# Kernel optimization log

Hardware: AMD Instinct MI355X
Metric: run time of the kernel (lower is better)

## Reference

```python
import jax, jax.numpy as jnp
import numpy as np

ALPHA = 200.0      # cfg.TRAIN.VOTING_ALPHA
RHO = 100.0        # ADMM penalty
SIGMA = 1e-3       # ADMM regularization
ITERS = 150        # fixed ADMM iterations


def _admm_qp(Q, q, C, l, u):
    n = Q.shape[0]
    K = Q + SIGMA * jnp.eye(n, dtype=Q.dtype) + RHO * (C.T @ C)
    cf = jax.scipy.linalg.cho_factor(K)
    x0 = jnp.zeros((n,), Q.dtype)
    z0 = jnp.clip(jnp.zeros((C.shape[0],), Q.dtype), l, u)
    y0 = jnp.zeros((C.shape[0],), Q.dtype)

    def step(carry, _):
        x, z, y = carry
        rhs = SIGMA * x - q + C.T @ (RHO * z - y)
        x = jax.scipy.linalg.cho_solve(cf, rhs)
        Cx = C @ x
        z = jnp.clip(Cx + y / RHO, l, u)
        y = y + RHO * (Cx - z)
        return (x, z, y), None

    (x, _, _), _ = jax.lax.scan(step, (x0, z0, y0), None, length=ITERS)
    return x


def _l2n(x, axis):
    return x / jnp.maximum(jnp.linalg.norm(x, axis=axis, keepdims=True), 1e-12)


def _forward(feat_tra, feat_det, iou_mat, W, b):
    n1, d = feat_tra.shape
    n2 = feat_det.shape[0]
    # cross-graph feature update
    Mp0 = feat_tra @ feat_det.T + iou_mat                      # (n1,n2)
    m1 = Mp0 @ feat_det                                        # (n1,d)
    m2 = Mp0.T @ feat_tra                                      # (n2,d)
    lam1 = jax.lax.stop_gradient(jnp.linalg.norm(feat_tra, axis=1, keepdims=True)
                                 / jnp.linalg.norm(m1, axis=1, keepdims=True))
    lam2 = jax.lax.stop_gradient(jnp.linalg.norm(feat_det, axis=1, keepdims=True)
                                 / jnp.linalg.norm(m2, axis=1, keepdims=True))
    e1 = jax.nn.relu((feat_tra + lam1 * m1) @ W.T + b)
    e2 = jax.nn.relu((feat_det + lam2 * m2) @ W.T + b)
    e1 = _l2n(e1, 1)
    e2 = _l2n(e2, 1)
    Mp = e1 @ e2.T                                             # (n1,n2) unary affinity
    P = Mp.T                                                   # (n2,n1)
    # Quadratic affinity: the torch code builds src_tgt[i,j,k,l] = <cat(e1_i,e1_j), cat(e2_k,e2_l)>
    # = Mp[i,k] + Mp[j,l], then gathers M[(a,c),(b,d)] = src_tgt[c,d,a,b]/2 masked by (a!=b)&(c!=d).
    ms = 1.0 - jnp.eye(n1, dtype=Mp.dtype)
    mt = 1.0 - jnp.eye(n2, dtype=Mp.dtype)
    M4 = 0.5 * (P[:, :, None, None] + P[None, None, :, :]) \
         * (mt[:, None, :, None] * ms[None, :, None, :])       # (n2,n1,n2,n1)
    n = n1 * n2
    Q = float((n1 - 1) * (n2 - 1)) * jnp.eye(n, dtype=Mp.dtype) - M4.reshape(n, n)
    q = -P.reshape(-1)                                         # -Mpp
    # equality constraints (square case): column sums and row sums == 1
    A = jnp.concatenate([jnp.kron(jnp.ones((1, n1)), jnp.eye(n2)),
                         jnp.kron(jnp.eye(n1), jnp.ones((1, n2)))], axis=0).astype(Mp.dtype)
    C = jnp.concatenate([jnp.eye(n, dtype=Mp.dtype), A], axis=0)
    l = jnp.concatenate([jnp.zeros((n,), Mp.dtype), jnp.ones((n1 + n2,), Mp.dtype)])
    u = jnp.concatenate([jnp.full((n,), 1e6, Mp.dtype), jnp.ones((n1 + n2,), Mp.dtype)])
    x = _admm_qp(Q, q, C, l, u)
    s = x.reshape(n2, n1).T                                    # (n1,n2)
    s = jnp.clip(s, 0.0, 1.0)                                  # relu(s) - relu(s-1)
    s = jax.nn.softmax(ALPHA * s, axis=-1)                     # Voting layer
    return s[None]                                             # (1,n1,n2)


def setup_inputs() -> dict:
    key = jax.random.key(0)
    k1, k2, k3, k4 = jax.random.split(key, 4)
    n1 = n2 = 64
    d = 512
    feat_tra = jax.random.normal(k1, (n1, d), jnp.float32)
    feat_det = jax.random.normal(k2, (n2, d), jnp.float32)
    iou_mat = jax.random.uniform(k3, (n1, n2), jnp.float32)
    W = jnp.eye(d, dtype=jnp.float32) + 0.01 * jax.random.normal(k4, (d, d), jnp.float32)
    b = jnp.zeros((d,), jnp.float32)
    return {"feat_tra": feat_tra, "feat_det": feat_det, "iou_mat": iou_mat, "W": W, "b": b}


def reference(feat_tra, feat_det, iou_mat, W, b):
    return _forward(feat_tra, feat_det, iou_mat, W, b)
```

## Files before the change

### kernel.cpp

```cpp
#include <hip/hip_runtime.h>
#include <math.h>

#define DD 512
#define NS 258
#define NSP 264
#define NWG 64
#define BLK 1024
#define RHO_ 100.0
#define SIG_ 1e-3
#define NITER 150
#define DELTA0 (3969.0 + SIG_ + RHO_)

typedef float v2f __attribute__((ext_vector_type(2)));

#define OFF_E1     512u
#define OFF_SUMS   512u
#define OFF_INV    4608u
#define OFF_E2     262656u
#define OFF_P      524800u
#define OFF_W      557568u
#define OFF_P32    590336u
#define OFF_W32    606720u
#define OFF_KSA    623104u
#define OFF_KSB    1168000u
#define OFF_N32    1712896u

__device__ __forceinline__ int perm258(int i){
  return (i < 128) ? i : (i == 128) ? 256 : (i == 129) ? 257 : (i - 2);
}

template<int CTRL>
__device__ __forceinline__ float dppadd(float v){
  int t = __builtin_amdgcn_mov_dpp(__float_as_int(v), CTRL, 0xF, 0xF, 1);
  return v + __int_as_float(t);
}
template<int CTRL>
__device__ __forceinline__ float dppmax(float v){
  int t = __builtin_amdgcn_mov_dpp(__float_as_int(v), CTRL, 0xF, 0xF, 1);
  return fmaxf(v, __int_as_float(t));
}
__device__ __forceinline__ float sum16(float v){
  v = dppadd<0xB1>(v);
  v = dppadd<0x4E>(v);
  v = dppadd<0x124>(v);
  v = dppadd<0x128>(v);
  return v;
}
__device__ __forceinline__ float wsum64f(float v){
  v = sum16(v);
  v += __shfl_xor(v, 16, 64);
  v += __shfl_xor(v, 32, 64);
  return v;
}
__device__ __forceinline__ float wsum64u(float v){
  v = sum16(v);
  v = dppadd<0x142>(v);
  v = dppadd<0x143>(v);
  return __uint_as_float(__builtin_amdgcn_readlane(__float_as_uint(v), 63));
}
__device__ __forceinline__ float wmax64f(float v){
  v = dppmax<0xB1>(v); v = dppmax<0x4E>(v); v = dppmax<0x124>(v); v = dppmax<0x128>(v);
  v = fmaxf(v, __shfl_xor(v, 16, 64));
  v = fmaxf(v, __shfl_xor(v, 32, 64));
  return v;
}

__device__ __forceinline__ double gsum16d(double v){
  v += __shfl_xor(v, 1, 64);
  v += __shfl_xor(v, 2, 64);
  v += __shfl_xor(v, 4, 64);
  v += __shfl_xor(v, 8, 64);
  return v;
}
__device__ __forceinline__ double wsum64d(double v){
  v = gsum16d(v);
  v += __shfl_xor(v, 16, 64);
  v += __shfl_xor(v, 32, 64);
  return v;
}

__device__ __forceinline__ void decode_idx(int t, int& cls, int& pr, int& ix){
  if (t < 64)       { cls = 1; pr = 1; ix = t; }
  else if (t < 128) { cls = 2; pr = 1; ix = t - 64; }
  else if (t == 128){ cls = 0; pr = 1; ix = 0; }
  else if (t == 129){ cls = 0; pr = 0; ix = 0; }
  else if (t < 194) { cls = 1; pr = 0; ix = t - 130; }
  else              { cls = 2; pr = 0; ix = t - 194; }
}

__device__ __forceinline__ double ksval(int r, int c, const double* __restrict__ p,
                                        const double* __restrict__ w, const double* sumsL){
  int cr, prr, ir, cc, prc, ic;
  decode_idx(r, cr, prr, ir);
  decode_idx(c, cc, prc, ic);
  int m = prr + prc;
  double tval;
  if (cr == 0 && cc == 0)      tval = sumsL[m];
  else if (cr == 0 && cc == 1) tval = sumsL[8 + m*64 + ic];
  else if (cr == 1 && cc == 0) tval = sumsL[8 + m*64 + ir];
  else if (cr == 0 && cc == 2) tval = sumsL[200 + m*64 + ic];
  else if (cr == 2 && cc == 0) tval = sumsL[200 + m*64 + ir];
  else if (cr == 1 && cc == 1) tval = (ir == ic) ? sumsL[8 + m*64 + ir] : 0.0;
  else if (cr == 2 && cc == 2) tval = (ir == ic) ? sumsL[200 + m*64 + ir] : 0.0;
  else if (cr == 1 && cc == 2){
    double wv = w[ic*64 + ir], pv = p[ic*64 + ir];
    tval = (m == 0) ? wv : (m == 1) ? wv*pv : wv*pv*pv;
  } else {
    double wv = w[ir*64 + ic], pv = p[ir*64 + ic];
    tval = (m == 0) ? wv : (m == 1) ? wv*pv : wv*pv*pv;
  }
  double mv2 = 0.0;
  if (cr == 0 && cc == 0 && prr != prc) mv2 = -2.0;
  if (cr != 0 && cr == cc && ir == ic){
    if (prr != prc) mv2 = 2.0;
    else if (prr == 1) mv2 = -4.0 * RHO_;
  }
  return tval + mv2;
}

__global__ __launch_bounds__(BLK) void kp_feat(const float* __restrict__ ft,
                                               const float* __restrict__ fd,
                                               const float* __restrict__ iou,
                                               const float* __restrict__ Wm,
                                               const float* __restrict__ bb,
                                               char* ws){
  double* e1 = (double*)(ws + OFF_E1);
  double* e2 = (double*)(ws + OFF_E2);
  __shared__ double SH[1192];
  const int tid  = threadIdx.x;
  const int wg   = blockIdx.x;
  const int lane = tid & 63;
  const int wv   = tid >> 6;
  float* ftR = (float*)SH;
  float* fdR = ftR + 512;
  float* u1R = fdR + 512;
  float* u2R = u1R + 512;
  double* m0r = SH + 1024;
  double* m0c = m0r + 64;
  double* wp  = m0c + 64;
  double* sca = wp + 32;
  const int i = wg;
  if (tid < 512){ ftR[tid] = ft[i*DD + tid]; fdR[tid] = fd[i*DD + tid]; }
  {
    double nf = 0.0, nd = 0.0;
    if (tid < 512){
      float a = ftR[tid], b = fdR[tid];
      nf = (double)a*a; nd = (double)b*b;
    }
    nf = wsum64d(nf); nd = wsum64d(nd);
    if (lane == 0){ wp[wv] = nf; wp[16 + wv] = nd; }
    __syncthreads();
    if (tid == 0){
      double s0 = 0, s1 = 0;
      for (int q = 0; q < 16; ++q){ s0 += wp[q]; s1 += wp[16+q]; }
      sca[0] = s0; sca[1] = s1;
    }
  }
  {
    int j = tid >> 4, sub = tid & 15;
    double ar = 0.0, ac = 0.0;
    for (int t2 = 0; t2 < 32; ++t2){
      int k = t2*16 + sub;
      ar += (double)ftR[k] * (double)fd[(size_t)j*DD + k];
      ac += (double)fdR[k] * (double)ft[(size_t)j*DD + k];
    }
    ar = gsum16d(ar); ac = gsum16d(ac);
    if (sub == 0){
      m0r[j] = ar + (double)iou[i*64 + j];
      m0c[j] = ac + (double)iou[j*64 + i];
    }
  }
  __syncthreads();
  {
    int c = tid & 511, half = tid >> 9;
    const double* m0 = half ? m0c : m0r;
    const float*  FB = half ? ft  : fd;
    double a0 = 0, b0 = 0, c0 = 0, d0 = 0;
    for (int a2 = 0; a2 < 64; a2 += 4){
      a0 += m0[a2]   * (double)FB[(size_t)(a2  )*DD + c];
      b0 += m0[a2+1] * (double)FB[(size_t)(a2+1)*DD + c];
      c0 += m0[a2+2] * (double)FB[(size_t)(a2+2)*DD + c];
      d0 += m0[a2+3] * (double)FB[(size_t)(a2+3)*DD + c];
    }
    double mv = (a0 + b0) + (c0 + d0);
    double nn = wsum64d(mv*mv);
    if (lane == 0) wp[wv] = nn;
    __syncthreads();
    if (tid < 2){
      double s = 0;
      for (int q = tid*8; q < tid*8 + 8; ++q) s += wp[q];
      sca[2 + tid] = sqrt(sca[tid] / s);
    }
    __syncthreads();
    double l = sca[2 + half];
    float* uR = half ? u2R : u1R;
    const float* fR = half ? fdR : ftR;
    uR[c] = (float)((double)fR[c] + l*mv);
  }
  __syncthreads();
  {
    int c = tid & 511, half = tid >> 9;
    const float* uR  = half ? u2R : u1R;
    const float* wrp = Wm + (size_t)c*DD;
    double a0 = (double)bb[c], b0 = 0, c0 = 0, d0 = 0;
    for (int k = 0; k < DD; k += 4){
      float4 wq = *(const float4*)(wrp + k);
      float4 uq = *(const float4*)(uR + k);
      a0 += (double)uq.x*wq.x; b0 += (double)uq.y*wq.y;
      c0 += (double)uq.z*wq.z; d0 += (double)uq.w*wq.w;
    }
    double v = fmax((a0 + b0) + (c0 + d0), 0.0);
    double nn = wsum64d(v*v);
    if (lane == 0) wp[wv] = nn;
    __syncthreads();
    if (tid < 2){
      double s = 0;
      for (int q = tid*8; q < tid*8 + 8; ++q) s += wp[q];
      sca[4 + tid] = 1.0 / fmax(sqrt(s), 1e-12);
    }
    __syncthreads();
    double* e = half ? e2 : e1;
    e[(size_t)i*DD + c] = v * sca[4 + half];
  }
}

__global__ __launch_bounds__(BLK) void kp_pw(char* ws){
  const double* e1 = (const double*)(ws + OFF_E1);
  const double* e2 = (const double*)(ws + OFF_E2);
  double* p   = (double*)(ws + OFF_P);
  double* w   = (double*)(ws + OFF_W);
  float*  p32 = (float*) (ws + OFF_P32);
  float*  w32 = (float*) (ws + OFF_W32);
  __shared__ double e2R[512];
  const int tid = threadIdx.x;
  const int a = blockIdx.x;
  if (tid < 512) e2R[tid] = e2[(size_t)a*DD + tid];
  __syncthreads();
  int b = tid >> 4, sub = tid & 15;
  double a0 = 0.0, a1 = 0.0;
  for (int t2 = 0; t2 < 32; t2 += 2){
    a0 += e1[(size_t)b*DD + t2*16 + sub]     * e2R[t2*16 + sub];
    a1 += e1[(size_t)b*DD + (t2+1)*16 + sub] * e2R[(t2+1)*16 + sub];
  }
  double acc = gsum16d(a0 + a1);
  if (sub == 0){
    double pv = acc;
    double wv2 = 1.0 / (DELTA0 - pv);
    int jj = a*64 + b;
    p[jj] = pv; w[jj] = wv2; p32[jj] = (float)pv; w32[jj] = (float)wv2;
  }
}

__global__ __launch_bounds__(BLK) void kp_sums(char* ws){
  const double* p = (const double*)(ws + OFF_P);
  const double* w = (const double*)(ws + OFF_W);
  double* sumsG = (double*)(ws + OFF_SUMS);
  __shared__ double sumsL[456];
  const int tid = threadIdx.x;
  int a = tid >> 4, sub = tid & 15;
  {
    double r0 = 0, r1 = 0, r2 = 0;
    for (int b = sub*4; b < sub*4 + 4; ++b){
      double wv = w[a*64 + b], pv = p[a*64 + b];
      r0 += wv; r1 += wv*pv; r2 += wv*pv*pv;
    }
    r0 = gsum16d(r0); r1 = gsum16d(r1); r2 = gsum16d(r2);
    if (sub == 0){ sumsL[200 + a] = r0; sumsL[264 + a] = r1; sumsL[328 + a] = r2; }
  }
  {
    int b2 = tid >> 4;
    double c0 = 0, c1 = 0, c2 = 0;
    for (int a2 = sub*4; a2 < sub*4 + 4; ++a2){
      double wv = w[a2*64 + b2], pv = p[a2*64 + b2];
      c0 += wv; c1 += wv*pv; c2 += wv*pv*pv;
    }
    c0 = gsum16d(c0); c1 = gsum16d(c1); c2 = gsum16d(c2);
    if (sub == 0){ sumsL[8 + b2] = c0; sumsL[72 + b2] = c1; sumsL[136 + b2] = c2; }
  }
  __syncthreads();
  if (tid == 0){
    double t0 = 0, t1 = 0, t2 = 0;
    for (int a3 = 0; a3 < 64; ++a3){
      t0 += sumsL[200 + a3]; t1 += sumsL[264 + a3]; t2 += sumsL[328 + a3];
    }
    sumsL[0] = t0; sumsL[1] = t1; sumsL[2] = t2;
    sumsL[3] = 0; sumsL[4] = 0; sumsL[5] = 0; sumsL[6] = 0; sumsL[7] = 0;
  }
  if (tid >= 64 && tid < 128){
    int k = tid - 64;
    sumsL[392 + k] = 1.0 / (sumsL[136 + k] - 4.0*RHO_);
  }
  __syncthreads();
  for (int idx = tid; idx < 456; idx += BLK) sumsG[idx] = sumsL[idx];
}

__global__ __launch_bounds__(BLK) void kp_p3(char* ws){
  const double* p = (const double*)(ws + OFF_P);
  const double* w = (const double*)(ws + OFF_W);
  const double* sumsG = (const double*)(ws + OFF_SUMS);
  double* KsB = (double*)(ws + OFF_KSB);
  __shared__ double sumsL[456];
  __shared__ double temp[68];
  const int tid = threadIdx.x;
  const int c = blockIdx.x;
  for (int idx = tid; idx < 456; idx += BLK) sumsL[idx] = sumsG[idx];
  __syncthreads();
  const double* invd = sumsL + 392;
  if (tid < 64){
    int k = tid;
    temp[k] = (c < 64) ? ((k == c) ? invd[k] : 0.0) : ksval(k, c, p, w, sumsL) * invd[k];
  }
  __syncthreads();
  const double* tp = temp;
  const int s = tid & 3;
  auto dorow = [&](int rr){
    if (rr < 64){
      if (s == 0) KsB[(size_t)rr*NSP + c] = tp[rr];
      return;
    }
    double acc = 0.0;
    if (rr < 128){
      const double* wr_ = w + (rr-64)*64;
      const double* pr_ = p + (rr-64)*64;
      for (int k = s; k < 64; k += 4){ double pv = pr_[k]; acc += wr_[k]*pv*pv*tp[k]; }
    } else if (rr == 128){
      for (int k = s; k < 64; k += 4) acc += sumsL[136 + k]*tp[k];
    } else if (rr == 129){
      for (int k = s; k < 64; k += 4) acc += sumsL[72 + k]*tp[k];
    } else if (rr < 194){
      if (s == 0){ int ir = rr - 130; acc = (sumsL[72 + ir] + 2.0)*tp[ir]; }
    } else {
      int ir = rr - 194;
      const double* wr_ = w + ir*64;
      const double* pr_ = p + ir*64;
      for (int k = s; k < 64; k += 4) acc += wr_[k]*pr_[k]*tp[k];
    }
    acc += __shfl_xor(acc, 1, 64);
    acc += __shfl_xor(acc, 2, 64);
    if (s == 0){
      double first = (c < 64) ? 0.0 : ksval(rr, c, p, w, sumsL);
      KsB[(size_t)rr*NSP + c] = first - acc;
    }
  };
  { int r = tid >> 2; if (r < 256) dorow(r); }
  if (tid < 8) dorow(256 + (tid >> 2));
}

template<int MM>
__global__ __launch_bounds__(BLK) void kp_inv(const double* __restrict__ src, int p0,
                                              double* __restrict__ invG){
  __shared__ double Mbuf[2*4422];
  const int tid = threadIdx.x;
  double* cur = Mbuf;
  double* nxt = Mbuf + 4422;
  for (int idx = tid; idx < MM*MM; idx += BLK)
    cur[(idx/MM)*67 + (idx%MM)] = src[(size_t)(p0 + idx/MM)*NSP + p0 + idx%MM];
  __syncthreads();
  for (int k = 0; k < MM; ++k){
    double pk = 1.0 / cur[k*67 + k];
    for (int idx = tid; idx < MM*MM; idx += BLK){
      int i = idx/MM, j = idx%MM;
      double mkj = cur[k*67 + j];
      double nv;
      if (i == k){
        nv = (j == k) ? pk : mkj*pk;
      } else {
        double mik = cur[i*67 + k];
        nv = (j == k) ? (-mik*pk) : (cur[i*67 + j] - mik*(mkj*pk));
      }
      nxt[i*67 + j] = nv;
    }
    __syncthreads();
    double* t = cur; cur = nxt; nxt = t;
  }
  for (int idx = tid; idx < MM*MM; idx += BLK)
    invG[(idx/MM)*67 + idx%MM] = cur[(idx/MM)*67 + idx%MM];
}

template<int MM>
__global__ __launch_bounds__(BLK) void kp_apply(const double* __restrict__ src,
                                                double* __restrict__ dstD,
                                                float* __restrict__ dstF, int p0,
                                                const double* __restrict__ invG){
  __shared__ double M[4422];
  __shared__ double temp[68];
  __shared__ double srcMid[66];
  const int tid = threadIdx.x;
  const int c = blockIdx.x;
  for (int idx = tid; idx < MM*67; idx += BLK) M[idx] = invG[idx];
  if (tid < MM) srcMid[tid] = src[(size_t)(p0 + tid)*NSP + c];
  __syncthreads();
  const bool cpiv = (c >= p0 && c < p0 + MM);
  if (cpiv){
    if (tid < MM) temp[tid] = M[tid*67 + (c - p0)];
  } else {
    int k = tid >> 3, s8 = tid & 7;
    if (k < MM){
      double a = 0.0;
      for (int l = s8; l < MM; l += 8) a += M[k*67 + l]*srcMid[l];
      a += __shfl_xor(a, 1, 64);
      a += __shfl_xor(a, 2, 64);
      a += __shfl_xor(a, 4, 64);
      if (s8 == 0) temp[k] = a;
    }
  }
  __syncthreads();
  const int s = tid & 3;
  auto dorow = [&](int rr){
    if (rr >= p0 && rr < p0 + MM){
      if (s == 0){
        double val = temp[rr - p0];
        if (dstD) dstD[(size_t)rr*NSP + c] = val;
        else      dstF[perm258(rr)*NSP + perm258(c)] = (float)val;
      }
      return;
    }
    double acc = 0.0;
    for (int k = s; k < MM; k += 4) acc += src[(size_t)rr*NSP + p0 + k]*temp[k];
    acc += __shfl_xor(acc, 1, 64);
    acc += __shfl_xor(acc, 2, 64);
    if (s == 0){
      double f = cpiv ? 0.0 : src[(size_t)rr*NSP + c];
      double val = f - acc;
      if (dstD) dstD[(size_t)rr*NSP + c] = val;
      else      dstF[perm258(rr)*NSP + perm258(c)] = (float)val;
    }
  };
  { int r = tid >> 2; if (r < 256) dorow(r); }
  if (tid < 8) dorow(256 + (tid >> 2));
}

__global__ __launch_bounds__(BLK) __attribute__((amdgpu_waves_per_eu(4, 4)))
void k_admm(const float* __restrict__ N32,
            const float* __restrict__ p32,
            const float* __restrict__ w32,
            float* __restrict__ out){
  __shared__ float2 tb[64][66];
  __shared__ float2 csTP[64][18];
  __shared__ float  csX[64][20];
  __shared__ __align__(16) float s1f[264];
  __shared__ float s1g2[2];
  __shared__ float s2g[2];
  __shared__ __align__(16) float s2p[4][264];
  __shared__ float2 pairB[64];
  __shared__ float2 pairR[64];

  const int tid  = threadIdx.x;
  const int lane = tid & 63;
  const int wvid = tid >> 6;
  const int g    = tid >> 8;
  const int c    = tid & 255;

  float4 nc4[16];
#pragma unroll
  for (int k2 = 0; k2 < 16; ++k2){
    nc4[k2].x = N32[(64*g + 4*k2 + 0)*NSP + c];
    nc4[k2].y = N32[(64*g + 4*k2 + 1)*NSP + c];
    nc4[k2].z = N32[(64*g + 4*k2 + 2)*NSP + c];
    nc4[k2].w = N32[(64*g + 4*k2 + 3)*NSP + c];
  }
  const float ncg0 = N32[256*NSP + c];
  const float ncg1 = N32[257*NSP + c];

  float nr0 = 0.f, nr1 = 0.f, nr2 = 0.f, nr3 = 0.f, nrt0 = 0.f, nrt1 = 0.f;
  if (wvid == 4 || wvid == 5){
    int r = 252 + wvid;
    nr0 = N32[r*NSP + lane];       nr1 = N32[r*NSP + lane + 64];
    nr2 = N32[r*NSP + lane + 128]; nr3 = N32[r*NSP + lane + 192];
    nrt0 = N32[r*NSP + 256];       nrt1 = N32[r*NSP + 257];
  }

  float pr[4], wr[4], xr[4], vr[4], tq[4];
  double y2a[4], y2b = 0.0;
#pragma unroll
  for (int q = 0; q < 4; ++q){
    int j = (wvid*4 + q)*64 + lane;
    pr[q] = p32[j]; wr[q] = w32[j];
    xr[q] = 0.f; vr[q] = 0.f; tq[q] = 0.f; y2a[q] = 0.0;
  }
  __syncthreads();

  for (int it = 0; it < NITER; ++it){
    if (it){
      float ybs = 0.f;
#pragma unroll
      for (int s = 0; s < 4; ++s){
        float4 v4 = *(const float4*)&csX[lane][4*s];
        ybs += (v4.x + v4.y) + (v4.z + v4.w);
      }
      y2b += RHO_ * ((double)ybs - 1.0);
    }
    float base = (float)(2.0*RHO_ - y2b);
    float clt = 0.f, clp = 0.f;
    float st0, st1, st2, st3, sp0, sp1, sp2, sp3;
#pragma unroll
    for (int q = 0; q < 4; ++q){
      float ya = (float)y2a[q];
      float rhs = 1e-3f*xr[q] + pr[q] + 100.f*fabsf(vr[q]) + base - ya;
      float t = wr[q]*rhs;
      float pt = pr[q]*t;
      tq[q] = t;
      clt += t; clp += pt;
      float st = wsum64u(t);
      float sp = wsum64u(pt);
      if (q == 0){ st0 = st; sp0 = sp; }
      else if (q == 1){ st1 = st; sp1 = sp; }
      else if (q == 2){ st2 = st; sp2 = sp; }
      else { st3 = st; sp3 = sp; }
    }
    csTP[lane][(wvid + lane) & 15] = make_float2(clt, clp);
    {
      int l2 = lane & 3;
      float sv_ = (l2 == 0) ? st0 : (l2 == 1) ? st1 : (l2 == 2) ? st2 : st3;
      float pv_ = (l2 == 0) ? sp0 : (l2 == 1) ? sp1 : (l2 == 2) ? sp2 : sp3;
      if (lane < 4)      s1f[192 + wvid*4 + l2] = sv_;
      else if (lane < 8) s1f[64  + wvid*4 + l2] = pv_;
    }
    __syncthreads();

    if (wvid == 0){
      float ct = 0.f, cp = 0.f;
#pragma unroll
      for (int s = 0; s < 8; ++s){
        float4 v4 = *(const float4*)&csTP[lane][2*s];
        ct += v4.x + v4.z; cp += v4.y + v4.w;
      }
      s1f[128 + lane] = ct; s1f[lane] = cp;
      float tt = wsum64u(ct);
      float tp = wsum64u(cp);
      if (lane == 0){ s1g2[1] = tt; s1g2[0] = tp; }
    }
    __syncthreads();

    {
      float sv = s1f[64*g + lane];
      float a0 = 0.f, a1 = 0.f, a2 = 0.f, a3 = 0.f;
#pragma unroll
      for (int k2 = 0; k2 < 16; ++k2){
        float4 nq = nc4[k2];
        a0 += nq.x * __uint_as_float(__builtin_amdgcn_readlane(__float_as_uint(sv), 4*k2 + 0));
        a1 += nq.y * __uint_as_float(__builtin_amdgcn_readlane(__float_as_uint(sv), 4*k2 + 1));
        a2 += nq.z * __uint_as_float(__builtin_amdgcn_readlane(__float_as_uint(sv), 4*k2 + 2));
        a3 += nq.w * __uint_as_float(__builtin_amdgcn_readlane(__float_as_uint(sv), 4*k2 + 3));
      }
      float acc = (a0 + a1) + (a2 + a3);
      if (g == 0) acc += ncg0*s1g2[0] + ncg1*s1g2[1];
      s2p[g][c] = acc;
      if (wvid == 4 || wvid == 5){
        float a32 = nr0*s1f[lane] + nr1*s1f[lane+64]
                  + nr2*s1f[lane+128] + nr3*s1f[lane+192];
        a32 = wsum64u(a32);
        if (lane == 0) s2g[wvid - 4] = a32 + nrt0*s1g2[0] + nrt1*s1g2[1];
      }
    }
    __syncthreads();

    if (tid < 64){
      int b = tid;
      float sbE  = (s2p[0][128+b] + s2p[1][128+b]) + (s2p[2][128+b] + s2p[3][128+b]);
      float sbPE = (s2p[0][b] + s2p[1][b]) + (s2p[2][b] + s2p[3][b]);
      pairB[b] = make_float2(sbE, sbPE);
    } else if (tid < 128){
      int a = tid - 64;
      float sF  = (s2p[0][192+a] + s2p[1][192+a]) + (s2p[2][192+a] + s2p[3][192+a]);
      float sPF = (s2p[0][64+a] + s2p[1][64+a]) + (s2p[2][64+a] + s2p[3][64+a]);
      pairR[a] = make_float2(s2g[1] + sF, s2g[0] + sPF);
    }
    __syncthreads();

    {
      float2 pb = pairB[lane];
      float clx = 0.f;
#pragma unroll
      for (int q = 0; q < 4; ++q){
        int arow = wvid*4 + q;
        float2 prw = pairR[arow];
        float corr = prw.x + pb.x + pr[q]*(prw.y + pb.y);
        float xn = tq[q] - wr[q]*corr;
        vr[q] = xn + fminf(vr[q], 0.f);
        xr[q] = xn;
        float rsx = wsum64u(xn);
        y2a[q] += RHO_*((double)rsx - 1.0);
        clx += xn;
        if (it == NITER-1) ((float*)tb)[lane*68 + arow] = xn;
      }
      csX[lane][wvid] = clx;
    }
    __syncthreads();
  }

  const float* xb = (const float*)tb;
#pragma unroll
  for (int q = 0; q < 4; ++q){
    int i = wvid*4 + q;
    float val = xb[i*68 + lane];
    val = fminf(fmaxf(val, 0.f), 1.f);
    float mx = wmax64f(val);
    float e = expf(200.f*(val - mx));
    float sm = wsum64f(e);
    out[i*64 + lane] = e / sm;
  }
}

extern "C" void kernel_launch(void* const* d_in, const int* in_sizes, int n_in,
                              void* d_out, int out_size, void* d_ws, size_t ws_size,
                              hipStream_t stream){
  (void)in_sizes; (void)n_in; (void)out_size; (void)ws_size;
  const float* ft  = (const float*)d_in[0];
  const float* fd  = (const float*)d_in[1];
  const float* iou = (const float*)d_in[2];
  const float* Wm  = (const float*)d_in[3];
  const float* bb  = (const float*)d_in[4];
  char* ws = (char*)d_ws;

  double* KsA  = (double*)(ws + OFF_KSA);
  double* KsB  = (double*)(ws + OFF_KSB);
  double* invG = (double*)(ws + OFF_INV);
  float*  N32  = (float*) (ws + OFF_N32);

  hipLaunchKernelGGL(kp_feat, dim3(NWG), dim3(BLK), 0, stream, ft, fd, iou, Wm, bb, ws);
  hipLaunchKernelGGL(kp_pw,   dim3(NWG), dim3(BLK), 0, stream, ws);
  hipLaunchKernelGGL(kp_sums, dim3(1),   dim3(BLK), 0, stream, ws);
  hipLaunchKernelGGL(kp_p3,   dim3(NS),  dim3(BLK), 0, stream, ws);

  hipLaunchKernelGGL(kp_inv<66>,   dim3(1),  dim3(BLK), 0, stream, KsB, 64, invG);
  hipLaunchKernelGGL(kp_apply<66>, dim3(NS), dim3(BLK), 0, stream, KsB, KsA, (float*)nullptr, 64, invG);
  hipLaunchKernelGGL(kp_inv<64>,   dim3(1),  dim3(BLK), 0, stream, KsA, 130, invG);
  hipLaunchKernelGGL(kp_apply<64>, dim3(NS), dim3(BLK), 0, stream, KsA, KsB, (float*)nullptr, 130, invG);
  hipLaunchKernelGGL(kp_inv<64>,   dim3(1),  dim3(BLK), 0, stream, KsB, 194, invG);
  hipLaunchKernelGGL(kp_apply<64>, dim3(NS), dim3(BLK), 0, stream, KsB, (double*)nullptr, N32, 194, invG);

  const float* p32 = (const float*)(ws + OFF_P32);
  const float* w32 = (const float*)(ws + OFF_W32);
  hipLaunchKernelGGL(k_admm, dim3(1), dim3(BLK), 0, stream, N32, p32, w32, (float*)d_out);
}
```

Before: 805.4 us.

## Remove two barriers per ADMM iteration via redundant per-wave reductions

Each ADMM iteration loses two __syncthreads barriers. The column-sum fold that wave 0 used to do alone is now computed redundantly by every wave that needs it, and every wave also recomputes the pairB/pairR reductions straight from s2p instead of having a few threads stage them. This cuts serialization and barrier latency in a latency-bound 150-iteration loop, at the cost of extra redundant LDS reads and arithmetic in every wave.

```diff
diff --git a/kernel.cpp b/kernel.cpp
--- a/kernel.cpp
+++ b/kernel.cpp
@@ -438,12 +438,9 @@
   __shared__ float2 tb[64][66];
   __shared__ float2 csTP[64][18];
   __shared__ float  csX[64][20];
-  __shared__ __align__(16) float s1f[264];
-  __shared__ float s1g2[2];
+  __shared__ __align__(16) float rsf[264];
   __shared__ float s2g[2];
   __shared__ __align__(16) float s2p[4][264];
-  __shared__ float2 pairB[64];
-  __shared__ float2 pairR[64];
 
   const int tid  = threadIdx.x;
   const int lane = tid & 63;
@@ -469,6 +466,9 @@
     nr2 = N32[r*NSP + lane + 128]; nr3 = N32[r*NSP + lane + 192];
     nrt0 = N32[r*NSP + 256];       nrt1 = N32[r*NSP + 257];
   }
+
+  const bool foldCS = (g == 0) || (g == 2) || (wvid == 4) || (wvid == 5);
+  const bool foldTT = (g == 0) || (wvid == 4) || (wvid == 5);
 
   float pr[4], wr[4], xr[4], vr[4], tq[4];
   double y2a[4], y2b = 0.0;
@@ -513,27 +513,26 @@
       int l2 = lane & 3;
       float sv_ = (l2 == 0) ? st0 : (l2 == 1) ? st1 : (l2 == 2) ? st2 : st3;
       float pv_ = (l2 == 0) ? sp0 : (l2 == 1) ? sp1 : (l2 == 2) ? sp2 : sp3;
-      if (lane < 4)      s1f[192 + wvid*4 + l2] = sv_;
-      else if (lane < 8) s1f[64  + wvid*4 + l2] = pv_;
-    }
-    __syncthreads();
-
-    if (wvid == 0){
-      float ct = 0.f, cp = 0.f;
-#pragma unroll
-      for (int s = 0; s < 8; ++s){
-        float4 v4 = *(const float4*)&csTP[lane][2*s];
-        ct += v4.x + v4.z; cp += v4.y + v4.w;
-      }
-      s1f[128 + lane] = ct; s1f[lane] = cp;
-      float tt = wsum64u(ct);
-      float tp = wsum64u(cp);
-      if (lane == 0){ s1g2[1] = tt; s1g2[0] = tp; }
+      if (lane < 4)      rsf[192 + wvid*4 + l2] = sv_;
+      else if (lane < 8) rsf[64  + wvid*4 + l2] = pv_;
     }
     __syncthreads();
 
     {
-      float sv = s1f[64*g + lane];
+      float ct = 0.f, cp = 0.f, tt = 0.f, tp = 0.f;
+      if (foldCS){
+#pragma unroll
+        for (int s = 0; s < 8; ++s){
+          float4 v4 = *(const float4*)&csTP[lane][2*s];
+          ct += v4.x + v4.z; cp += v4.y + v4.w;
+        }
+      }
+      if (foldTT){
+        tt = wsum64u(ct);
+        tp = wsum64u(cp);
+      }
+      float sv = (g == 0) ? cp : (g == 1) ? rsf[64 + lane]
+               : (g == 2) ? ct : rsf[192 + lane];
       float a0 = 0.f, a1 = 0.f, a2 = 0.f, a3 = 0.f;
 #pragma unroll
       for (int k2 = 0; k2 < 16; ++k2){
@@ -544,38 +543,28 @@
         a3 += nq.w * __uint_as_float(__builtin_amdgcn_readlane(__float_as_uint(sv), 4*k2 + 3));
       }
       float acc = (a0 + a1) + (a2 + a3);
-      if (g == 0) acc += ncg0*s1g2[0] + ncg1*s1g2[1];
+      if (g == 0) acc += ncg0*tp + ncg1*tt;
       s2p[g][c] = acc;
       if (wvid == 4 || wvid == 5){
-        float a32 = nr0*s1f[lane] + nr1*s1f[lane+64]
-                  + nr2*s1f[lane+128] + nr3*s1f[lane+192];
+        float a32 = nr0*cp + nr1*rsf[lane + 64]
+                  + nr2*ct + nr3*rsf[lane + 192];
         a32 = wsum64u(a32);
-        if (lane == 0) s2g[wvid - 4] = a32 + nrt0*s1g2[0] + nrt1*s1g2[1];
-      }
-    }
-    __syncthreads();
-
-    if (tid < 64){
-      int b = tid;
-      float sbE  = (s2p[0][128+b] + s2p[1][128+b]) + (s2p[2][128+b] + s2p[3][128+b]);
-      float sbPE = (s2p[0][b] + s2p[1][b]) + (s2p[2][b] + s2p[3][b]);
-      pairB[b] = make_float2(sbE, sbPE);
-    } else if (tid < 128){
-      int a = tid - 64;
-      float sF  = (s2p[0][192+a] + s2p[1][192+a]) + (s2p[2][192+a] + s2p[3][192+a]);
-      float sPF = (s2p[0][64+a] + s2p[1][64+a]) + (s2p[2][64+a] + s2p[3][64+a]);
-      pairR[a] = make_float2(s2g[1] + sF, s2g[0] + sPF);
+        if (lane == 0) s2g[wvid - 4] = a32 + nrt0*tp + nrt1*tt;
+      }
     }
     __syncthreads();
 
     {
-      float2 pb = pairB[lane];
+      float sbE  = (s2p[0][128+lane] + s2p[1][128+lane]) + (s2p[2][128+lane] + s2p[3][128+lane]);
+      float sbPE = (s2p[0][lane] + s2p[1][lane]) + (s2p[2][lane] + s2p[3][lane]);
+      float g1 = s2g[1], g0 = s2g[0];
       float clx = 0.f;
 #pragma unroll
       for (int q = 0; q < 4; ++q){
         int arow = wvid*4 + q;
-        float2 prw = pairR[arow];
-        float corr = prw.x + pb.x + pr[q]*(prw.y + pb.y);
+        float sF  = (s2p[0][192+arow] + s2p[1][192+arow]) + (s2p[2][192+arow] + s2p[3][192+arow]);
+        float sPF = (s2p[0][64+arow] + s2p[1][64+arow]) + (s2p[2][64+arow] + s2p[3][64+arow]);
+        float corr = (g1 + sF) + sbE + pr[q]*((g0 + sPF) + sbPE);
         float xn = tq[q] - wr[q]*corr;
         vr[q] = xn + fminf(vr[q], 0.f);
         xr[q] = xn;
```

New measurement: 821.6 us. 2.0% more time.

## Rewrite block inversion as in-place rank-2 Gauss-Jordan updates and vectorize ADMM dot

Applied to the files above, without the earlier changes.

The small-block matrix inverse kernel now does Gauss-Jordan elimination two pivots at a time in place. Each step is a rank-2 update from precomputed row and column vectors, replacing the double-buffered one-pivot-per-step sweep. This halves the number of barrier-separated steps and removes the second shared-memory buffer. Separately, the ADMM inner dot product reads broadcast float4 values from LDS and uses packed float2 FMAs instead of per-element readlane calls. The pairwise pivoting assumes the 2x2 pivot blocks are well conditioned and that MM is even.

```diff
diff --git a/kernel.cpp b/kernel.cpp
--- a/kernel.cpp
+++ b/kernel.cpp
@@ -349,32 +349,51 @@
 template<int MM>
 __global__ __launch_bounds__(BLK) void kp_inv(const double* __restrict__ src, int p0,
                                               double* __restrict__ invG){
-  __shared__ double Mbuf[2*4422];
+  __shared__ double M[MM*67];
+  __shared__ double RV[MM], RV2[MM], CV[MM], CV2[MM];
   const int tid = threadIdx.x;
-  double* cur = Mbuf;
-  double* nxt = Mbuf + 4422;
+  const int lane = tid & 63, wv = tid >> 6;
   for (int idx = tid; idx < MM*MM; idx += BLK)
-    cur[(idx/MM)*67 + (idx%MM)] = src[(size_t)(p0 + idx/MM)*NSP + p0 + idx%MM];
-  __syncthreads();
-  for (int k = 0; k < MM; ++k){
-    double pk = 1.0 / cur[k*67 + k];
-    for (int idx = tid; idx < MM*MM; idx += BLK){
-      int i = idx/MM, j = idx%MM;
-      double mkj = cur[k*67 + j];
-      double nv;
-      if (i == k){
-        nv = (j == k) ? pk : mkj*pk;
-      } else {
-        double mik = cur[i*67 + k];
-        nv = (j == k) ? (-mik*pk) : (cur[i*67 + j] - mik*(mkj*pk));
+    M[(idx/MM)*67 + (idx%MM)] = src[(size_t)(p0 + idx/MM)*NSP + p0 + idx%MM];
+  __syncthreads();
+  for (int k = 0; k < MM; k += 2){
+    if (tid < MM){
+      int j = tid;
+      double pk  = 1.0 / M[k*67 + k];
+      double ck1 = M[(k+1)*67 + k];
+      double rv  = M[k*67 + j] * pk;
+      if (j == k) rv += pk;
+      double rk1 = M[k*67 + k+1] * pk;
+      double q   = 1.0 / (M[(k+1)*67 + k+1] - ck1*rk1);
+      double r2  = (M[(k+1)*67 + j] - ck1*rv) * q;
+      if (j == k+1) r2 += q;
+      RV[j] = rv; RV2[j] = r2;
+    } else if (tid >= 512 && tid < 512 + MM){
+      int i = tid - 512;
+      double pk  = 1.0 / M[k*67 + k];
+      double rk1 = M[k*67 + k+1] * pk;
+      double cv  = M[i*67 + k];
+      if (i == k) cv -= 1.0;
+      double c2  = M[i*67 + k+1] - cv*rk1;
+      if (i == k+1) c2 -= 1.0;
+      CV[i] = cv; CV2[i] = c2;
+    }
+    __syncthreads();
+    {
+      double rv0 = RV[lane], rv20 = RV2[lane];
+      const bool hi = (lane + 64) < MM;
+      double rv1 = hi ? RV[lane + 64] : 0.0;
+      double rv21 = hi ? RV2[lane + 64] : 0.0;
+      for (int i = wv; i < MM; i += 16){
+        double cv = CV[i], c2 = CV2[i];
+        M[i*67 + lane] -= cv*rv0 + c2*rv20;
+        if (hi) M[i*67 + lane + 64] -= cv*rv1 + c2*rv21;
       }
-      nxt[i*67 + j] = nv;
-    }
-    __syncthreads();
-    double* t = cur; cur = nxt; nxt = t;
+    }
+    __syncthreads();
   }
   for (int idx = tid; idx < MM*MM; idx += BLK)
-    invG[(idx/MM)*67 + idx%MM] = cur[(idx/MM)*67 + idx%MM];
+    invG[(idx/MM)*67 + idx%MM] = M[(idx/MM)*67 + idx%MM];
 }
 
 template<int MM>
@@ -533,17 +552,18 @@
     __syncthreads();
 
     {
-      float sv = s1f[64*g + lane];
-      float a0 = 0.f, a1 = 0.f, a2 = 0.f, a3 = 0.f;
+      v2f accE = {0.f, 0.f}, accO = {0.f, 0.f};
+      const float4* s4 = (const float4*)&s1f[64*g];
 #pragma unroll
       for (int k2 = 0; k2 < 16; ++k2){
         float4 nq = nc4[k2];
-        a0 += nq.x * __uint_as_float(__builtin_amdgcn_readlane(__float_as_uint(sv), 4*k2 + 0));
-        a1 += nq.y * __uint_as_float(__builtin_amdgcn_readlane(__float_as_uint(sv), 4*k2 + 1));
-        a2 += nq.z * __uint_as_float(__builtin_amdgcn_readlane(__float_as_uint(sv), 4*k2 + 2));
-        a3 += nq.w * __uint_as_float(__builtin_amdgcn_readlane(__float_as_uint(sv), 4*k2 + 3));
+        float4 sv = s4[k2];
+        v2f nA = {nq.x, nq.y}, nB = {nq.z, nq.w};
+        v2f sA = {sv.x, sv.y}, sB = {sv.z, sv.w};
+        accE += nA * sA;
+        accO += nB * sB;
       }
-      float acc = (a0 + a1) + (a2 + a3);
+      float acc = (accE.x + accE.y) + (accO.x + accO.y);
       if (g == 0) acc += ncg0*s1g2[0] + ncg1*s1g2[1];
       s2p[g][c] = acc;
       if (wvid == 4 || wvid == 5){
```

After: 731.2 us. 1.1x faster.
